# Kernel optimization log

Hardware: AMD Instinct MI355X
Metric: run time of the kernel (lower is better)

Reference implementation:

```python
import jax, jax.numpy as jnp
import numpy as np


def position_encoding(sent_len, embed_size):
    # PE from the source: encoding[i-1,j-1] = (i - d/2) * (j - L/2), i in 1..d, j in 1..L
    # then 1 + 4*enc/d/L, transposed to [L, d]
    i = jnp.arange(1, embed_size + 1, dtype=jnp.float32)  # embed index
    j = jnp.arange(1, sent_len + 1, dtype=jnp.float32)    # word index
    enc = (i[:, None] - embed_size / 2.0) * (j[None, :] - sent_len / 2.0)  # [d, L]
    enc = 1.0 + 4.0 * enc / embed_size / sent_len
    return enc.T  # [L, d]


def setup_inputs() -> dict:
    key = jax.random.key(0)
    k1, k2, k3, k4 = jax.random.split(key, 4)
    B, M, L, V, D, HOPS = 256, 50, 50, 50257, 128, 3
    x_e = jax.random.randint(k1, (B, M, L), 0, V, dtype=jnp.int32)
    x_q = jax.random.randint(k2, (B, L), 0, V, dtype=jnp.int32)
    # hops+1 tied embedding tables: A0, C0(=A1), C1(=A2), C2
    emb = jax.random.normal(k3, (HOPS + 1, V, D), dtype=jnp.float32) * 0.1
    W = jax.random.normal(k4, (D, V), dtype=jnp.float32)
    return {"x_e": x_e, "x_q": x_q, "emb": emb, "W": W}


def reference(x_e, x_q, emb, W):
    hops = emb.shape[0] - 1
    D = emb.shape[-1]
    Lq = x_q.shape[-1]
    Le = x_e.shape[-1]
    pe_q = position_encoding(Lq, D)  # [Lq, D]
    pe_e = position_encoding(Le, D)  # [Le, D]

    # query embedding with position encoding, summed over words -> u: [B, D]
    u = jnp.sum(emb[0][x_q] * pe_q, axis=1)

    for i in range(hops):
        # memory embeddings (input side A_i and output side C_i = emb[i+1])
        m_a = jnp.sum(emb[i][x_e] * pe_e, axis=2)      # [B, M, D]
        p = jax.nn.softmax(jnp.einsum("bmd,bd->bm", m_a, u), axis=-1)  # [B, M]
        m_c = jnp.sum(emb[i + 1][x_e] * pe_e, axis=2)  # [B, M, D]
        o = jnp.einsum("bm,bmd->bd", p, m_c)           # [B, D]
        u = o + u

    logits = u @ W  # [B, V]
    return jax.nn.softmax(logits, axis=-1)
```

## Files before the change

### kernel.cpp

```cpp
#include <hip/hip_runtime.h>
#include <hip/hip_bf16.h>
#include <hip/hip_fp16.h>
#include <math.h>

#define PB   256
#define PM   50
#define PL   50
#define PV   50257
#define PD   128
#define PBM  (PB * PM)
#define TS   ((size_t)PV * PD)
#define PEC  0.000625f
#define NT   786
#define PVP  (NT * 64)
#define NCONV 786
#define NCH  16
#define CHW  3142
#define UPB  50

typedef _Float16 f16x8 __attribute__((ext_vector_type(8)));
typedef float    f32x4 __attribute__((ext_vector_type(4)));

__global__ __launch_bounds__(256) void k_sortconv(const int* __restrict__ xe,
                                                  const float* __restrict__ W,
                                                  unsigned* __restrict__ skey,
                                                  unsigned char* __restrict__ ucnt,
                                                  _Float16* __restrict__ Wt) {
    const int t = threadIdx.x;

    if (blockIdx.x < NCONV) {
        __shared__ float ls[PD][20];
        const bool edge = (blockIdx.x == NCONV - 1);
        #pragma unroll 1
        for (int p = 0; p < 4; ++p) {
            const int c0 = blockIdx.x * 64 + p * 16;
            #pragma unroll
            for (int i = 0; i < 2; ++i) {
                const int e  = t + i * 256;
                const int kk = e >> 2, c4 = (e & 3) * 4;
                const int gc = c0 + c4;
                f32x4 v;
                if (!edge || gc + 3 < PV) {
                    v = *reinterpret_cast<const f32x4*>(W + (size_t)kk * PV + gc);
                } else {
                    v.x = (gc + 0 < PV) ? W[(size_t)kk * PV + gc + 0] : 0.f;
                    v.y = (gc + 1 < PV) ? W[(size_t)kk * PV + gc + 1] : 0.f;
                    v.z = (gc + 2 < PV) ? W[(size_t)kk * PV + gc + 2] : 0.f;
                    v.w = (gc + 3 < PV) ? W[(size_t)kk * PV + gc + 3] : 0.f;
                }
                *reinterpret_cast<f32x4*>(&ls[kk][c4]) = v;
            }
            __syncthreads();
            {
                const int c = t >> 4, k0 = (t & 15) * 8;
                f16x8 v;
                #pragma unroll
                for (int j = 0; j < 8; ++j) v[j] = (_Float16)ls[k0 + j][c];
                *reinterpret_cast<f16x8*>(Wt + (size_t)(c0 + c) * PD + k0) = v;
            }
            __syncthreads();
        }
        return;
    }

    const int wv   = t >> 6;
    const int lane = t & 63;
    const int bm   = (blockIdx.x - NCONV) * 4 + wv;

    unsigned key = 0xFFFFFFFFu;
    if (lane < PL)
        key = ((unsigned)xe[(size_t)bm * PL + lane] << 6) | (unsigned)lane;

    #pragma unroll
    for (int k = 2; k <= 64; k <<= 1) {
        #pragma unroll
        for (int j = k >> 1; j > 0; j >>= 1) {
            const unsigned other = (unsigned)__shfl_xor((int)key, j);
            const bool up      = ((lane & k) == 0);
            const bool keepMin = (((lane & j) == 0) == up);
            const unsigned mn = key < other ? key : other;
            const unsigned mx = key < other ? other : key;
            key = keepMin ? mn : mx;
        }
    }
    if (lane < PL) skey[(size_t)bm * PL + lane] = key;

    const int ci = (int)((key >> 6) / (unsigned)CHW);
    #pragma unroll
    for (int c = 0; c < NCH; ++c) {
        const unsigned long long m = __ballot(lane < PL && ci == c);
        if (lane == c) ucnt[bm * NCH + c] = (unsigned char)__popcll(m);
    }
}

__global__ __launch_bounds__(512, 8) void k_gatherp(
        const unsigned* __restrict__ skey,
        const unsigned char* __restrict__ ucnt,
        const float* __restrict__ emb,
        float* __restrict__ Mw) {
    const int b    = blockIdx.x;
    const int x    = b & 7;
    const int k    = x >> 1;
    const int half = x & 1;
    const int slot = b >> 3;
    const int bm0  = half * 6400 + slot * UPB;

    const int t    = threadIdx.x;
    const int wv   = t >> 6;
    const int lane = t & 63;
    const int sub  = lane >> 5;
    const int d4   = (lane & 31) * 4;

    __shared__ unsigned      skeys[UPB][PL];
    __shared__ unsigned char scnt[UPB][NCH];

    for (int i = t; i < UPB * PL; i += 512)
        ((unsigned*)skeys)[i] = skey[(size_t)bm0 * PL + i];
    if (t < UPB * NCH / 4)
        ((unsigned*)scnt)[t] = ((const unsigned*)(ucnt + bm0 * NCH))[t];
    __syncthreads();

    const float* tab = emb + (size_t)k * TS;
    const float dd0 = (float)(d4 + 0) - 63.0f;
    const float dd1 = (float)(d4 + 1) - 63.0f;
    const float dd2 = (float)(d4 + 2) - 63.0f;
    const float dd3 = (float)(d4 + 3) - 63.0f;

    f32x4 acc[7];
    int   cur[7];
    #pragma unroll
    for (int i = 0; i < 7; ++i) {
        acc[i] = (f32x4){0.f, 0.f, 0.f, 0.f};
        cur[i] = 0;
    }

    #pragma unroll 1
    for (int c = 0; c < NCH; ++c) {
        #pragma unroll
        for (int i = 0; i < 7; ++i) {
            const int u = wv + 8 * i;
            if (u < UPB) {
                const int n    = (int)scnt[u][c];
                const int base = cur[i];
                f32x4 a = acc[i];
                for (int j = sub; j < n; j += 2) {
                    const unsigned key = skeys[u][base + j];
                    const int   l  = (int)(key & 63u);
                    const f32x4 v  = *reinterpret_cast<const f32x4*>(
                        tab + (size_t)(key >> 6) * PD + d4);
                    const float fl = PEC * ((float)l - 24.0f);
                    a.x += (1.0f + fl * dd0) * v.x;
                    a.y += (1.0f + fl * dd1) * v.y;
                    a.z += (1.0f + fl * dd2) * v.z;
                    a.w += (1.0f + fl * dd3) * v.w;
                }
                acc[i] = a;
                cur[i] = base + n;
            }
        }
    }

    #pragma unroll
    for (int i = 0; i < 7; ++i) {
        const int u = wv + 8 * i;
        f32x4 o;
        o.x = __shfl_down(acc[i].x, 32);
        o.y = __shfl_down(acc[i].y, 32);
        o.z = __shfl_down(acc[i].z, 32);
        o.w = __shfl_down(acc[i].w, 32);
        if (u < UPB && sub == 0) {
            const f32x4 s = acc[i] + o;
            *reinterpret_cast<f32x4*>(
                Mw + ((size_t)k * PBM + bm0 + u) * PD + d4) = s;
        }
    }
}

__global__ __launch_bounds__(1024) void k_hops(const int* __restrict__ xq,
                                               const float* __restrict__ emb,
                                               const float* __restrict__ Mw,
                                               _Float16* __restrict__ uh) {
    const int b = blockIdx.x;
    const int t = threadIdx.x;
    const int g = t >> 7;
    const int d = t & 127;

    __shared__ float us[PD];
    __shared__ float ps[64];
    __shared__ float red[8][PD];
    __shared__ int   sidx[PL];

    if (t < PL) sidx[t] = xq[(size_t)b * PL + t];
    __syncthreads();

    {
        const float dd = (float)d - 63.0f;
        float acc = 0.f;
        for (int l = g; l < PL; l += 8)
            acc += (1.0f + PEC * dd * ((float)l - 24.0f)) *
                   emb[(size_t)sidx[l] * PD + d];
        red[g][d] = acc;
    }
    __syncthreads();
    if (t < PD) {
        float s = red[0][t];
        #pragma unroll
        for (int i = 1; i < 8; ++i) s += red[i][t];
        us[t] = s;
    }
    __syncthreads();

    const int lane = t & 63;
    const int wave = t >> 6;

    for (int hop = 0; hop < 3; ++hop) {
        const float* Ma = Mw + ((size_t)hop * PBM + (size_t)b * PM) * PD;
        const float* Mc = Ma + (size_t)PBM * PD;

        for (int m = wave; m < PM; m += 16) {
            const float* row = Ma + (size_t)m * PD;
            float part = row[lane] * us[lane] + row[lane + 64] * us[lane + 64];
            #pragma unroll
            for (int off = 32; off > 0; off >>= 1)
                part += __shfl_down(part, off);
            if (lane == 0) ps[m] = part;
        }
        __syncthreads();

        if (wave == 0) {
            float s = (lane < PM) ? ps[lane] : -INFINITY;
            float mx = s;
            #pragma unroll
            for (int off = 32; off > 0; off >>= 1)
                mx = fmaxf(mx, __shfl_xor(mx, off));
            float e = (lane < PM) ? __expf(s - mx) : 0.f;
            float sm = e;
            #pragma unroll
            for (int off = 32; off > 0; off >>= 1)
                sm += __shfl_xor(sm, off);
            if (lane < PM) ps[lane] = e / sm;
        }
        __syncthreads();

        {
            float o = 0.f;
            for (int m = g; m < PM; m += 8)
                o += ps[m] * Mc[(size_t)m * PD + d];
            red[g][d] = o;
        }
        __syncthreads();
        if (t < PD) {
            float s = red[0][t];
            #pragma unroll
            for (int i = 1; i < 8; ++i) s += red[i][t];
            us[t] += s;
        }
        __syncthreads();
    }

    if (t < PD) uh[(size_t)b * PD + t] = (_Float16)us[t];
}

__global__ __launch_bounds__(128) void k_gemm_exp(const _Float16* __restrict__ uh,
                                                  const _Float16* __restrict__ Wt,
                                                  _Float16* __restrict__ Eh,
                                                  float* __restrict__ part) {
    const int tile    = blockIdx.x;
    const int colBase = tile * 64;
    const int w       = threadIdx.x >> 6;
    const int l       = threadIdx.x & 63;
    const int lrow    = l & 15;
    const int lk      = (l >> 4) * 8;
    const int rb0     = blockIdx.y * 128;
    const int rowBase = rb0 + w * 64;

    __shared__ _Float16 es[128][72];

    f32x4 acc[4][4];
    #pragma unroll
    for (int i = 0; i < 4; ++i)
        #pragma unroll
        for (int j = 0; j < 4; ++j)
            acc[i][j] = (f32x4){0.f, 0.f, 0.f, 0.f};

    #pragma unroll
    for (int ks = 0; ks < 4; ++ks) {
        const int k0 = ks * 32 + lk;
        f16x8 a[4], bfr[4];
        #pragma unroll
        for (int mi = 0; mi < 4; ++mi)
            a[mi] = *reinterpret_cast<const f16x8*>(
                uh + (size_t)(rowBase + mi * 16 + lrow) * PD + k0);
        #pragma unroll
        for (int ni = 0; ni < 4; ++ni)
            bfr[ni] = *reinterpret_cast<const f16x8*>(
                Wt + (size_t)(colBase + ni * 16 + lrow) * PD + k0);
        #pragma unroll
        for (int mi = 0; mi < 4; ++mi)
            #pragma unroll
            for (int ni = 0; ni < 4; ++ni)
                acc[mi][ni] = __builtin_amdgcn_mfma_f32_16x16x32_f16(
                    a[mi], bfr[ni], acc[mi][ni], 0, 0, 0);
    }

    const int rquad = (l >> 4) * 4;
    #pragma unroll
    for (int mi = 0; mi < 4; ++mi) {
        #pragma unroll
        for (int q = 0; q < 4; ++q) {
            const int row   = rowBase + mi * 16 + rquad + q;
            const int row_l = row - rb0;
            float v[4];
            float mx = -INFINITY;
            #pragma unroll
            for (int j = 0; j < 4; ++j) {
                const int col = colBase + j * 16 + lrow;
                v[j] = (col < PV) ? acc[mi][j][q] : -INFINITY;
                mx = fmaxf(mx, v[j]);
            }
            #pragma unroll
            for (int msk = 1; msk < 16; msk <<= 1)
                mx = fmaxf(mx, __shfl_xor(mx, msk));
            float se = 0.f;
            #pragma unroll
            for (int j = 0; j < 4; ++j) {
                const float e = __expf(v[j] - mx);
                se += e;
                es[row_l][j * 16 + lrow] = (_Float16)e;
            }
            #pragma unroll
            for (int msk = 1; msk < 16; msk <<= 1)
                se += __shfl_xor(se, msk);
            if (lrow == 0) {
                part[((size_t)tile * PB + row) * 2 + 0] = mx;
                part[((size_t)tile * PB + row) * 2 + 1] = se;
            }
        }
    }
    __syncthreads();

    #pragma unroll
    for (int i = 0; i < 8; ++i) {
        const int ch    = threadIdx.x + i * 128;
        const int row_l = ch >> 3, cq = ch & 7;
        const f16x8 v = *reinterpret_cast<const f16x8*>(&es[row_l][cq * 8]);
        *reinterpret_cast<f16x8*>(
            Eh + (size_t)(rb0 + row_l) * PVP + colBase + cq * 8) = v;
    }
}

__global__ __launch_bounds__(512) void k_scale(const _Float16* __restrict__ Eh,
                                               const float* __restrict__ part,
                                               float* __restrict__ out) {
    const int b = blockIdx.x;
    const int t = threadIdx.x;
    __shared__ float sc[NT];
    __shared__ float wm[8], ws[8];

    float M = -INFINITY, S = 0.f;
    for (int tile = t; tile < NT; tile += 512) {
        const float m = part[((size_t)tile * PB + b) * 2 + 0];
        const float s = part[((size_t)tile * PB + b) * 2 + 1];
        const float nM = fmaxf(M, m);
        S = S * __expf(M - nM) + s * __expf(m - nM);
        M = nM;
    }
    #pragma unroll
    for (int off = 32; off > 0; off >>= 1) {
        const float m2 = __shfl_xor(M, off);
        const float s2 = __shfl_xor(S, off);
        const float nM = fmaxf(M, m2);
        S = S * __expf(M - nM) + s2 * __expf(m2 - nM);
        M = nM;
    }
    if ((t & 63) == 0) { wm[t >> 6] = M; ws[t >> 6] = S; }
    __syncthreads();
    M = -INFINITY; S = 0.f;
    #pragma unroll
    for (int i = 0; i < 8; ++i) {
        const float m = wm[i], s = ws[i];
        const float nM = fmaxf(M, m);
        S = S * __expf(M - nM) + s * __expf(m - nM);
        M = nM;
    }
    const float rinv = 1.0f / S;

    for (int tile = t; tile < NT; tile += 512)
        sc[tile] = __expf(part[((size_t)tile * PB + b) * 2 + 0] - M) * rinv;
    __syncthreads();

    const _Float16* erow = Eh + (size_t)b * PVP;
    float*          orow = out + (size_t)b * PV;

    const int NP = PV >> 1;
    for (int i = t; i < NP; i += 512) {
        const int c = 2 * i;
        const unsigned u = *reinterpret_cast<const unsigned*>(erow + c);
        const _Float16 e0 = ((const _Float16*)&u)[0];
        const _Float16 e1 = ((const _Float16*)&u)[1];
        const float s0 = sc[c >> 6];
        orow[c]     = (float)e0 * s0;
        orow[c + 1] = (float)e1 * s0;
    }
    if (t == 0)
        orow[PV - 1] = (float)erow[PV - 1] * sc[(PV - 1) >> 6];
}

extern "C" void kernel_launch(void* const* d_in, const int* in_sizes, int n_in,
                              void* d_out, int out_size, void* d_ws, size_t ws_size,
                              hipStream_t stream) {
    const int*   x_e = (const int*)d_in[0];
    const int*   x_q = (const int*)d_in[1];
    const float* emb = (const float*)d_in[2];
    const float* W   = (const float*)d_in[3];
    float*       out = (float*)d_out;
    (void)n_in; (void)in_sizes; (void)out_size; (void)ws_size;

    char* p = (char*)d_ws;
    float*         M_ws = (float*)p;           p += (size_t)4 * PBM * PD * 4;
    _Float16*      uh   = (_Float16*)p;        p += (size_t)PB * PD * 2;
    _Float16*      Wt   = (_Float16*)p;        p += (size_t)PVP * PD * 2;
    float*         part = (float*)p;           p += (size_t)NT * PB * 2 * 4;
    _Float16*      Eh   = (_Float16*)p;        p += (size_t)PB * PVP * 2;
    unsigned*      skey = (unsigned*)p;        p += (size_t)PBM * PL * 4;
    unsigned char* ucnt = (unsigned char*)p;

    k_sortconv<<<dim3(NCONV + PBM / 4), dim3(256), 0, stream>>>(
        x_e, W, skey, ucnt, Wt);
    k_gatherp <<<dim3(1024),            dim3(512), 0, stream>>>(
        skey, ucnt, emb, M_ws);
    k_hops    <<<dim3(PB),              dim3(1024), 0, stream>>>(x_q, emb, M_ws, uh);
    k_gemm_exp<<<dim3(NT, 2),           dim3(128),  0, stream>>>(uh, Wt, Eh, part);
    k_scale   <<<dim3(PB),              dim3(512),  0, stream>>>(Eh, part, out);
}
```

Before: 163.4 us.

## Fuse token sort and W conversion into the gather kernel

Merges the sort/convert kernel into the gather kernel. Each gather block now bitonic-sorts its own token keys in shared memory instead of going through a global skey/ucnt round trip, and extra blocks in the same launch do the W-to-fp16 transpose with wider 32-column tiles. The chunk count drops from 16 to 8, and the inner gather loop is unrolled by two to issue more independent loads. This removes one kernel launch and the intermediate global traffic. In exchange, every one of the four table blocks that shares a bm group redoes the same sort, and the block uses more shared memory, which may reduce occupancy.

After: 246.8 us. 1.51x slower.

```diff
diff --git a/kernel.cpp b/kernel.cpp
--- a/kernel.cpp
+++ b/kernel.cpp
@@ -13,34 +13,37 @@
 #define PEC  0.000625f
 #define NT   786
 #define PVP  (NT * 64)
-#define NCONV 786
-#define NCH  16
-#define CHW  3142
+#define NCH  8
+#define CHW  6283
 #define UPB  50
+#define NGB  1024
+#define NCV  393
 
 typedef _Float16 f16x8 __attribute__((ext_vector_type(8)));
 typedef float    f32x4 __attribute__((ext_vector_type(4)));
 
-__global__ __launch_bounds__(256) void k_sortconv(const int* __restrict__ xe,
-                                                  const float* __restrict__ W,
-                                                  unsigned* __restrict__ skey,
-                                                  unsigned char* __restrict__ ucnt,
-                                                  _Float16* __restrict__ Wt) {
+__global__ __launch_bounds__(512, 8) void k_gather_all(
+        const int* __restrict__ xe, const float* __restrict__ emb,
+        const float* __restrict__ W, float* __restrict__ Mw,
+        _Float16* __restrict__ Wt) {
     const int t = threadIdx.x;
 
-    if (blockIdx.x < NCONV) {
-        __shared__ float ls[PD][20];
-        const bool edge = (blockIdx.x == NCONV - 1);
+    __shared__ unsigned      skeys[UPB][PL];
+    __shared__ unsigned char scnt[UPB][NCH];
+    __shared__ float         ls[PD][36];
+
+    if (blockIdx.x >= NGB) {
+        const int cb = (blockIdx.x - NGB) * 128;
         #pragma unroll 1
         for (int p = 0; p < 4; ++p) {
-            const int c0 = blockIdx.x * 64 + p * 16;
+            const int c0 = cb + p * 32;
             #pragma unroll
             for (int i = 0; i < 2; ++i) {
-                const int e  = t + i * 256;
-                const int kk = e >> 2, c4 = (e & 3) * 4;
+                const int e  = t + i * 512;
+                const int kk = e >> 3, c4 = (e & 7) * 4;
                 const int gc = c0 + c4;
                 f32x4 v;
-                if (!edge || gc + 3 < PV) {
+                if (gc + 3 < PV) {
                     v = *reinterpret_cast<const f32x4*>(W + (size_t)kk * PV + gc);
                 } else {
                     v.x = (gc + 0 < PV) ? W[(size_t)kk * PV + gc + 0] : 0.f;
@@ -63,41 +66,6 @@
         return;
     }
 
-    const int wv   = t >> 6;
-    const int lane = t & 63;
-    const int bm   = (blockIdx.x - NCONV) * 4 + wv;
-
-    unsigned key = 0xFFFFFFFFu;
-    if (lane < PL)
-        key = ((unsigned)xe[(size_t)bm * PL + lane] << 6) | (unsigned)lane;
-
-    #pragma unroll
-    for (int k = 2; k <= 64; k <<= 1) {
-        #pragma unroll
-        for (int j = k >> 1; j > 0; j >>= 1) {
-            const unsigned other = (unsigned)__shfl_xor((int)key, j);
-            const bool up      = ((lane & k) == 0);
-            const bool keepMin = (((lane & j) == 0) == up);
-            const unsigned mn = key < other ? key : other;
-            const unsigned mx = key < other ? other : key;
-            key = keepMin ? mn : mx;
-        }
-    }
-    if (lane < PL) skey[(size_t)bm * PL + lane] = key;
-
-    const int ci = (int)((key >> 6) / (unsigned)CHW);
-    #pragma unroll
-    for (int c = 0; c < NCH; ++c) {
-        const unsigned long long m = __ballot(lane < PL && ci == c);
-        if (lane == c) ucnt[bm * NCH + c] = (unsigned char)__popcll(m);
-    }
-}
-
-__global__ __launch_bounds__(512, 8) void k_gatherp(
-        const unsigned* __restrict__ skey,
-        const unsigned char* __restrict__ ucnt,
-        const float* __restrict__ emb,
-        float* __restrict__ Mw) {
     const int b    = blockIdx.x;
     const int x    = b & 7;
     const int k    = x >> 1;
@@ -105,19 +73,36 @@
     const int slot = b >> 3;
     const int bm0  = half * 6400 + slot * UPB;
 
-    const int t    = threadIdx.x;
     const int wv   = t >> 6;
     const int lane = t & 63;
     const int sub  = lane >> 5;
     const int d4   = (lane & 31) * 4;
 
-    __shared__ unsigned      skeys[UPB][PL];
-    __shared__ unsigned char scnt[UPB][NCH];
-
-    for (int i = t; i < UPB * PL; i += 512)
-        ((unsigned*)skeys)[i] = skey[(size_t)bm0 * PL + i];
-    if (t < UPB * NCH / 4)
-        ((unsigned*)scnt)[t] = ((const unsigned*)(ucnt + bm0 * NCH))[t];
+    for (int u = wv; u < UPB; u += 8) {
+        const int bm = bm0 + u;
+        unsigned key = 0xFFFFFFFFu;
+        if (lane < PL)
+            key = ((unsigned)xe[(size_t)bm * PL + lane] << 6) | (unsigned)lane;
+        #pragma unroll
+        for (int kk = 2; kk <= 64; kk <<= 1) {
+            #pragma unroll
+            for (int j = kk >> 1; j > 0; j >>= 1) {
+                const unsigned other = (unsigned)__shfl_xor((int)key, j);
+                const bool up      = ((lane & kk) == 0);
+                const bool keepMin = (((lane & j) == 0) == up);
+                const unsigned mn = key < other ? key : other;
+                const unsigned mx = key < other ? other : key;
+                key = keepMin ? mn : mx;
+            }
+        }
+        if (lane < PL) skeys[u][lane] = key;
+        const int ci = (int)((key >> 6) / (unsigned)CHW);
+        #pragma unroll
+        for (int c = 0; c < NCH; ++c) {
+            const unsigned long long m = __ballot(lane < PL && ci == c);
+            if (lane == c) scnt[u][c] = (unsigned char)__popcll(m);
+        }
+    }
     __syncthreads();
 
     const float* tab = emb + (size_t)k * TS;
@@ -143,16 +128,30 @@
                 const int n    = (int)scnt[u][c];
                 const int base = cur[i];
                 f32x4 a = acc[i];
-                for (int j = sub; j < n; j += 2) {
-                    const unsigned key = skeys[u][base + j];
-                    const int   l  = (int)(key & 63u);
-                    const f32x4 v  = *reinterpret_cast<const f32x4*>(
-                        tab + (size_t)(key >> 6) * PD + d4);
-                    const float fl = PEC * ((float)l - 24.0f);
-                    a.x += (1.0f + fl * dd0) * v.x;
-                    a.y += (1.0f + fl * dd1) * v.y;
-                    a.z += (1.0f + fl * dd2) * v.z;
-                    a.w += (1.0f + fl * dd3) * v.w;
+                int j = sub;
+                for (; j + 2 < n; j += 4) {
+                    const unsigned k1 = skeys[u][base + j];
+                    const unsigned k2 = skeys[u][base + j + 2];
+                    const f32x4 v1 = *reinterpret_cast<const f32x4*>(
+                        tab + (size_t)(k1 >> 6) * PD + d4);
+                    const f32x4 v2 = *reinterpret_cast<const f32x4*>(
+                        tab + (size_t)(k2 >> 6) * PD + d4);
+                    const float fl1 = PEC * ((float)(int)(k1 & 63u) - 24.0f);
+                    const float fl2 = PEC * ((float)(int)(k2 & 63u) - 24.0f);
+                    a.x += (1.0f + fl1 * dd0) * v1.x + (1.0f + fl2 * dd0) * v2.x;
+                    a.y += (1.0f + fl1 * dd1) * v1.y + (1.0f + fl2 * dd1) * v2.y;
+                    a.z += (1.0f + fl1 * dd2) * v1.z + (1.0f + fl2 * dd2) * v2.z;
+                    a.w += (1.0f + fl1 * dd3) * v1.w + (1.0f + fl2 * dd3) * v2.w;
+                }
+                if (j < n) {
+                    const unsigned k1 = skeys[u][base + j];
+                    const f32x4 v1 = *reinterpret_cast<const f32x4*>(
+                        tab + (size_t)(k1 >> 6) * PD + d4);
+                    const float fl1 = PEC * ((float)(int)(k1 & 63u) - 24.0f);
+                    a.x += (1.0f + fl1 * dd0) * v1.x;
+                    a.y += (1.0f + fl1 * dd1) * v1.y;
+                    a.z += (1.0f + fl1 * dd2) * v1.z;
+                    a.w += (1.0f + fl1 * dd3) * v1.w;
                 }
                 acc[i] = a;
                 cur[i] = base + n;
@@ -417,19 +416,15 @@
     (void)n_in; (void)in_sizes; (void)out_size; (void)ws_size;
 
     char* p = (char*)d_ws;
-    float*         M_ws = (float*)p;           p += (size_t)4 * PBM * PD * 4;
-    _Float16*      uh   = (_Float16*)p;        p += (size_t)PB * PD * 2;
-    _Float16*      Wt   = (_Float16*)p;        p += (size_t)PVP * PD * 2;
-    float*         part = (float*)p;           p += (size_t)NT * PB * 2 * 4;
-    _Float16*      Eh   = (_Float16*)p;        p += (size_t)PB * PVP * 2;
-    unsigned*      skey = (unsigned*)p;        p += (size_t)PBM * PL * 4;
-    unsigned char* ucnt = (unsigned char*)p;
-
-    k_sortconv<<<dim3(NCONV + PBM / 4), dim3(256), 0, stream>>>(
-        x_e, W, skey, ucnt, Wt);
-    k_gatherp <<<dim3(1024),            dim3(512), 0, stream>>>(
-        skey, ucnt, emb, M_ws);
-    k_hops    <<<dim3(PB),              dim3(1024), 0, stream>>>(x_q, emb, M_ws, uh);
-    k_gemm_exp<<<dim3(NT, 2),           dim3(128),  0, stream>>>(uh, Wt, Eh, part);
-    k_scale   <<<dim3(PB),              dim3(512),  0, stream>>>(Eh, part, out);
+    float*    M_ws = (float*)p;                p += (size_t)4 * PBM * PD * 4;
+    _Float16* uh   = (_Float16*)p;             p += (size_t)PB * PD * 2;
+    _Float16* Wt   = (_Float16*)p;             p += (size_t)PVP * PD * 2;
+    float*    part = (float*)p;                p += (size_t)NT * PB * 2 * 4;
+    _Float16* Eh   = (_Float16*)p;
+
+    k_gather_all<<<dim3(NGB + NCV), dim3(512),  0, stream>>>(
+        x_e, emb, W, M_ws, Wt);
+    k_hops    <<<dim3(PB),    dim3(1024), 0, stream>>>(x_q, emb, M_ws, uh);
+    k_gemm_exp<<<dim3(NT, 2), dim3(128),  0, stream>>>(uh, Wt, Eh, part);
+    k_scale   <<<dim3(PB),    dim3(512),  0, stream>>>(Eh, part, out);
 }
```
